# Optimization experiments

Hardware: AMD Instinct MI355X
Metric: run time of the kernel (lower is better)

Reference implementation:

```python
import jax, jax.numpy as jnp
import numpy as np

T0 = 16
EPS = 1.1920929e-07  # torch fp32 finfo eps used by F.rms_norm default

def rmsnorm(v):
    return v * jax.lax.rsqrt(jnp.mean(v * v, axis=-1, keepdims=True) + EPS)

def apply_rotary_emb(x, cos, sin):
    # x: (B, S, H, C); rotate-half style as in source
    d = x.shape[-1] // 2
    x1, x2 = x[..., :d], x[..., d:]
    return jnp.concatenate([x1 * cos + x2 * sin, -x1 * sin + x2 * cos], axis=-1)

def setup_inputs():
    key = jax.random.key(0)
    ks = jax.random.split(key, 8)
    B, T, C, H = 8, 8192, 128, 8
    S = (T0 // 4) * T0 + 1  # 64 selected tokens + 1 sink = 65
    x = jax.random.normal(ks[0], (B, T, C), jnp.float32)
    # RoPE tables over the sink-augmented attention sequence, head_dim/2 = 64
    inv = 1.0 / (10000.0 ** (jnp.arange(C // 2, dtype=jnp.float32) / (C // 2)))
    ang = jnp.arange(S, dtype=jnp.float32)[:, None] * inv[None, :]
    cos = jnp.cos(ang)[None, :, None, :]  # (1, 65, 1, 64)
    sin = jnp.sin(ang)[None, :, None, :]
    sink = 0.02 * jax.random.normal(ks[1], (1, H, C), jnp.float32)
    W_qkvg = 0.02 * jax.random.normal(ks[2], (4 * C * H, C), jnp.float32)
    patch_w = 0.02 * jax.random.normal(ks[3], (T0 * C,), jnp.float32)
    W_out = 0.02 * jax.random.normal(ks[4], (C, H * C), jnp.float32)
    tao = jnp.array([1.2, 1.2], jnp.float32)
    return {"x": x, "cos": cos, "sin": sin, "sink": sink, "W_qkvg": W_qkvg,
            "patch_w": patch_w, "W_out": W_out, "tao": tao}

def reference(x, cos, sin, sink, W_qkvg, patch_w, W_out, tao):
    B, T, C = x.shape
    H = sink.shape[1]
    Np = T // T0  # T chosen as multiple of T0, so pad P = 0
    # --- patch scoring + topk patch selection (patch_toks) ---
    xp = x.reshape(B, Np, T0 * C)
    score = jax.nn.softmax(rmsnorm(xp) @ patch_w, axis=-1)  # (B, Np)
    _, I = jax.lax.top_k(score, T0 // 4)                    # top 4 patches
    I = jnp.sort(I, axis=-1)                                # (B, 4)
    # --- qkvg projection over ALL tokens, then patch-flattened chunk ---
    qkvg = x @ W_qkvg.T                                     # (B, T, 4*C*H)
    qkvg_p = qkvg.reshape(B, Np, 4 * T0 * C * H)
    n = T0 * C * H
    q_p = qkvg_p[..., 0 * n:1 * n]
    k_p = qkvg_p[..., 1 * n:2 * n]
    v_p = qkvg_p[..., 2 * n:3 * n]
    g_p = qkvg_p[..., 3 * n:4 * n]
    def gather(p):  # (B, Np, n) -> (B, 4*T0, H, C) via selected patches
        return jnp.take_along_axis(p, I[:, :, None], axis=1).reshape(B, -1, H, C)
    q, k, v, g = gather(q_p), gather(k_p), gather(v_p), gather(g_p)
    # --- sink token prepend ---
    s = jnp.broadcast_to(sink[:, None], (B, 1, H, C))
    q = jnp.concatenate([s, q], axis=1)  # (B, 65, H, C)
    k = jnp.concatenate([s, k], axis=1)
    v = jnp.concatenate([s, v], axis=1)
    # --- RoPE + RMSNorm + learned temperatures ---
    q = rmsnorm(apply_rotary_emb(q, cos, sin)) * tao[0]
    k = rmsnorm(apply_rotary_emb(k, cos, sin)) * tao[1]
    # --- causal SDPA (scale 1/sqrt(C)), drop sink row ---
    S = q.shape[1]
    att = jnp.einsum('bshc,bthc->bhst', q, k) / jnp.sqrt(jnp.float32(C))
    causal = jnp.tril(jnp.ones((S, S), dtype=bool))
    att = jax.nn.softmax(jnp.where(causal, att, -jnp.inf), axis=-1)
    y = jnp.einsum('bhst,bthc->bshc', att, v)[:, 1:]  # (B, 64, H, C)
    # --- sigmoid gating + output projection ---
    y = y * jax.nn.sigmoid(g)
    return y.reshape(B, y.shape[1], H * C) @ W_out.T  # (B, 64, C)
```

## Files before the change

kernel.cpp:

```cpp
#include <hip/hip_runtime.h>
#include <hip/hip_bf16.h>

#define EPSR 1.1920929e-07f

#define OFF_SCORE 0LL
#define OFF_I     4096LL
#define OFF_WQT   8192LL
#define OFF_WO4   532480LL
#define OFF_SEL   663552LL
#define OFF_YG    4757504LL

__device__ __forceinline__ bool is_bf16_in(const void* tao) {
    unsigned int w = *(const unsigned int*)tao;
    return (w >> 16) == (w & 0xffffu);
}

__device__ __forceinline__ float ldin(const void* p, long long i, bool bf) {
    if (bf) return __uint_as_float(((unsigned int)(((const unsigned short*)p)[i])) << 16);
    return ((const float*)p)[i];
}

__device__ __forceinline__ float4 ldin4(const void* p, long long i, bool bf) {
    if (bf) {
        ushort4 u = ((const ushort4*)p)[i >> 2];
        return make_float4(__uint_as_float((unsigned int)u.x << 16),
                           __uint_as_float((unsigned int)u.y << 16),
                           __uint_as_float((unsigned int)u.z << 16),
                           __uint_as_float((unsigned int)u.w << 16));
    }
    return ((const float4*)p)[i >> 2];
}

__global__ __launch_bounds__(256) void k_prep_score(const void* Wq, const void* Wo,
                                                    const void* x, const void* pw,
                                                    const void* tao, float* ws) {
    bool bf = is_bf16_in(tao);
    __shared__ float tile[16448];
    int tid = threadIdx.x;
    if (blockIdx.x < 1024) {
        int lane = tid & 63, wid = tid >> 6;
        int patch = blockIdx.x * 4 + wid;
        long long base = (long long)patch * 2048;
        float ss = 0.f, dt = 0.f;
        #pragma unroll
        for (int i = 0; i < 8; i++) {
            int e = i * 256 + lane * 4;
            float4 v = ldin4(x, base + e, bf);
            float4 w = ldin4(pw, e, bf);
            ss += v.x * v.x + v.y * v.y + v.z * v.z + v.w * v.w;
            dt += v.x * w.x + v.y * w.y + v.z * w.z + v.w * w.w;
        }
        #pragma unroll
        for (int o = 32; o; o >>= 1) { ss += __shfl_xor(ss, o); dt += __shfl_xor(dt, o); }
        if (lane == 0) ws[OFF_SCORE + patch] = dt * rsqrtf(ss * (1.f / 2048.f) + EPSR);
    } else if (blockIdx.x < 1088) {
        float* WqT = ws + OFF_WQT;
        int j0 = (blockIdx.x - 1024) * 64;
        #pragma unroll
        for (int rep = 0; rep < 8; rep++) {
            int jr = rep * 8 + (tid >> 5);
            int c4 = (tid & 31) * 4;
            float4 v = ldin4(Wq, ((long long)(j0 + jr)) * 128 + c4, bf);
            float* t = &tile[jr * 129 + c4];
            t[0] = v.x; t[1] = v.y; t[2] = v.z; t[3] = v.w;
        }
        __syncthreads();
        #pragma unroll
        for (int rep = 0; rep < 8; rep++) {
            int c = rep * 16 + (tid >> 4);
            int jq = (tid & 15) * 4;
            float4 v = make_float4(tile[jq * 129 + c], tile[(jq + 1) * 129 + c],
                                   tile[(jq + 2) * 129 + c], tile[(jq + 3) * 129 + c]);
            *(float4*)&WqT[c * 4096 + j0 + jq] = v;
        }
    } else {
        float* Wo4 = ws + OFF_WO4;
        int co0 = (blockIdx.x - 1088) * 16;
        #pragma unroll
        for (int rep = 0; rep < 16; rep++) {
            float4 v = ldin4(Wo, ((long long)(co0 + rep)) * 1024 + tid * 4, bf);
            *(float4*)&tile[rep * 1028 + tid * 4] = v;
        }
        __syncthreads();
        #pragma unroll
        for (int rep = 0; rep < 16; rep++) {
            int idx = rep * 256 + tid;
            int fg = idx >> 4, co = idx & 15;
            float4 v = *(const float4*)&tile[co * 1028 + fg * 4];
            *(float4*)&Wo4[(fg * 128 + co0 + co) * 4] = v;
        }
    }
}

__global__ __launch_bounds__(64) void k_top4(float* ws) {
    const float* score = ws + OFF_SCORE;
    int* I = (int*)(ws + OFF_I);
    int b = blockIdx.x, lane = threadIdx.x;
    const float4* sp = (const float4*)(score + b * 512);
    float4 a = sp[lane * 2], c = sp[lane * 2 + 1];
    float v[8];
    v[0] = a.x; v[1] = a.y; v[2] = a.z; v[3] = a.w;
    v[4] = c.x; v[5] = c.y; v[6] = c.z; v[7] = c.w;
    int win[4];
    #pragma unroll
    for (int k = 0; k < 4; k++) {
        float bm = v[0]; int bi = 0;
        #pragma unroll
        for (int i = 1; i < 8; i++) if (v[i] > bm) { bm = v[i]; bi = i; }
        int gi = lane * 8 + bi;
        #pragma unroll
        for (int o = 32; o; o >>= 1) {
            float om = __shfl_xor(bm, o); int oi = __shfl_xor(gi, o);
            if (om > bm || (om == bm && oi < gi)) { bm = om; gi = oi; }
        }
        win[k] = gi;
        if ((gi >> 3) == lane) v[gi & 7] = -INFINITY;
    }
    if (lane == 0) {
        int a0 = win[0], a1 = win[1], a2 = win[2], a3 = win[3], tmp;
        if (a0 > a1) { tmp = a0; a0 = a1; a1 = tmp; }
        if (a2 > a3) { tmp = a2; a2 = a3; a3 = tmp; }
        if (a0 > a2) { tmp = a0; a0 = a2; a2 = tmp; }
        if (a1 > a3) { tmp = a1; a1 = a3; a3 = tmp; }
        if (a1 > a2) { tmp = a1; a1 = a2; a2 = tmp; }
        I[b * 4 + 0] = a0; I[b * 4 + 1] = a1; I[b * 4 + 2] = a2; I[b * 4 + 3] = a3;
    }
}

__global__ __launch_bounds__(128) void k_qkvg(const void* x, const void* tao, float* ws) {
    bool bf = is_bf16_in(tao);
    const int* I = (const int*)(ws + OFF_I);
    int blk = blockIdx.x;
    int jc = blk & 15, bp = blk >> 4;
    int b = bp >> 2;
    __shared__ float4 xs4[512];
    int tid = threadIdx.x;
    int tok0 = I[bp] * 16;
    long long xbase = ((long long)(b * 8192 + tok0)) * 128;
    for (int i = tid; i < 512; i += 128)
        xs4[i] = ldin4(x, xbase + i * 4, bf);
    __syncthreads();
    int ts = tid >> 6, jx = tid & 63;
    const float4* WqT4 = (const float4*)(ws + OFF_WQT);
    int wcol = jc * 64 + jx;
    float4 acc[8];
    #pragma unroll
    for (int t = 0; t < 8; t++) acc[t] = make_float4(0.f, 0.f, 0.f, 0.f);
    for (int c4 = 0; c4 < 32; c4++) {
        float4 w0 = WqT4[(c4 * 4 + 0) * 1024 + wcol];
        float4 w1 = WqT4[(c4 * 4 + 1) * 1024 + wcol];
        float4 w2 = WqT4[(c4 * 4 + 2) * 1024 + wcol];
        float4 w3 = WqT4[(c4 * 4 + 3) * 1024 + wcol];
        #pragma unroll
        for (int t = 0; t < 8; t++) {
            float4 xv = xs4[(ts * 8 + t) * 32 + c4];
            acc[t].x += xv.x * w0.x + xv.y * w1.x + xv.z * w2.x + xv.w * w3.x;
            acc[t].y += xv.x * w0.y + xv.y * w1.y + xv.z * w2.y + xv.w * w3.y;
            acc[t].z += xv.x * w0.z + xv.y * w1.z + xv.z * w2.z + xv.w * w3.z;
            acc[t].w += xv.x * w0.w + xv.y * w1.w + xv.z * w2.w + xv.w * w3.w;
        }
    }
    float4* sel4 = (float4*)(ws + OFF_SEL);
    #pragma unroll
    for (int t = 0; t < 8; t++)
        sel4[(bp * 16 + ts * 8 + t) * 1024 + wcol] = acc[t];
}

__global__ __launch_bounds__(512, 2) void k_fused(const void* sink, const void* cosp, const void* sinp,
                                                  const void* tao, float* ws) {
    bool bf = is_bf16_in(tao);
    const float* sel = ws + OFF_SEL;
    float* yg = ws + OFF_YG;
    int b = blockIdx.x >> 3, h = blockIdx.x & 7;
    int tid = threadIdx.x, lane = tid & 63, wid = tid >> 6;
    __shared__ float qs[65 * 132];
    __shared__ float ks[65 * 132];
    __shared__ float vs[65 * 132];
    __shared__ float att[65 * 68];
    float tao0 = ldin(tao, 0, bf), tao1 = ldin(tao, 1, bf);

    for (int s = wid; s < 65; s += 8) {
        float cs = ldin(cosp, s * 64 + lane, bf);
        float sn = ldin(sinp, s * 64 + lane, bf);
        #pragma unroll
        for (int which = 0; which < 3; which++) {
            float r1, r2;
            if (s == 0) {
                r1 = ldin(sink, h * 128 + lane, bf);
                r2 = ldin(sink, h * 128 + lane + 64, bf);
            } else {
                int r = s - 1, p = r >> 4, sl = r & 15;
                int tl = which * 4 + (sl >> 2);
                long long sbase = (((long long)(b * 4 + p) * 16 + tl) * 4096) + (sl & 3) * 1024 + h * 128;
                r1 = sel[sbase + lane];
                r2 = sel[sbase + lane + 64];
            }
            float o1, o2;
            if (which < 2) {
                o1 = r1 * cs + r2 * sn;
                o2 = -r1 * sn + r2 * cs;
                float ssum = o1 * o1 + o2 * o2;
                #pragma unroll
                for (int o = 32; o; o >>= 1) ssum += __shfl_xor(ssum, o);
                float sc = rsqrtf(ssum * (1.f / 128.f) + EPSR) * (which == 0 ? tao0 : tao1);
                o1 *= sc; o2 *= sc;
            } else {
                o1 = r1; o2 = r2;
            }
            float* dst = (which == 0 ? qs : which == 1 ? ks : vs);
            dst[s * 132 + lane] = o1;
            dst[s * 132 + lane + 64] = o2;
        }
    }
    __syncthreads();

    for (int tile = tid; tile < 561; tile += 512) {
        int u = tile, sT = 0;
        while (u >= sT + 1) { u -= sT + 1; sT++; }
        int tT = u;
        int s0 = sT * 2, t0 = tT * 2;
        const float* q0 = &qs[s0 * 132];
        const float* q1 = &qs[(s0 + 1 > 64 ? 64 : s0 + 1) * 132];
        const float* k0 = &ks[t0 * 132];
        const float* k1 = &ks[(t0 + 1 > 64 ? 64 : t0 + 1) * 132];
        float a00 = 0.f, a01 = 0.f, a10 = 0.f, a11 = 0.f;
        #pragma unroll 4
        for (int c = 0; c < 128; c += 4) {
            float4 qa = *(const float4*)(q0 + c);
            float4 qb = *(const float4*)(q1 + c);
            float4 ka = *(const float4*)(k0 + c);
            float4 kb = *(const float4*)(k1 + c);
            a00 += qa.x * ka.x + qa.y * ka.y + qa.z * ka.z + qa.w * ka.w;
            a01 += qa.x * kb.x + qa.y * kb.y + qa.z * kb.z + qa.w * kb.w;
            a10 += qb.x * ka.x + qb.y * ka.y + qb.z * ka.z + qb.w * ka.w;
            a11 += qb.x * kb.x + qb.y * kb.y + qb.z * kb.z + qb.w * kb.w;
        }
        const float scale = 0.08838834764831845f;
        if (t0 <= s0)                          att[s0 * 68 + t0] = a00 * scale;
        if (t0 + 1 <= s0)                      att[s0 * 68 + t0 + 1] = a01 * scale;
        if (s0 + 1 <= 64 && t0 <= s0 + 1)      att[(s0 + 1) * 68 + t0] = a10 * scale;
        if (s0 + 1 <= 64 && t0 + 1 <= s0 + 1)  att[(s0 + 1) * 68 + t0 + 1] = a11 * scale;
    }
    __syncthreads();

    for (int s = wid; s < 65; s += 8) {
        float x1 = (lane <= s) ? __expf(att[s * 68 + lane]) : 0.f;
        float x2 = (lane == 0 && s == 64) ? __expf(att[s * 68 + 64]) : 0.f;
        float sum = x1 + x2;
        #pragma unroll
        for (int o = 32; o; o >>= 1) sum += __shfl_xor(sum, o);
        float inv = 1.f / sum;
        att[s * 68 + lane] = x1 * inv;
        if (lane < 4) att[s * 68 + 64 + lane] = (lane == 0) ? x2 * inv : 0.f;
    }
    __syncthreads();

    {
        int rt = tid >> 4, ct = tid & 15;
        int c0 = ct * 8;
        float acc[2][8];
        #pragma unroll
        for (int i = 0; i < 2; i++)
            #pragma unroll
            for (int j = 0; j < 8; j++) acc[i][j] = 0.f;
        const float* ar[2];
        #pragma unroll
        for (int i = 0; i < 2; i++) ar[i] = &att[(1 + rt * 2 + i) * 68];
        for (int t4 = 0; t4 < 64; t4 += 4) {
            float aw[2][4];
            #pragma unroll
            for (int i = 0; i < 2; i++) *(float4*)aw[i] = *(const float4*)(ar[i] + t4);
            #pragma unroll
            for (int j = 0; j < 4; j++) {
                const float* vp = &vs[(t4 + j) * 132 + c0];
                float4 v1 = *(const float4*)vp;
                float4 v2 = *(const float4*)(vp + 4);
                #pragma unroll
                for (int i = 0; i < 2; i++) {
                    float a = aw[i][j];
                    acc[i][0] += a * v1.x; acc[i][1] += a * v1.y;
                    acc[i][2] += a * v1.z; acc[i][3] += a * v1.w;
                    acc[i][4] += a * v2.x; acc[i][5] += a * v2.y;
                    acc[i][6] += a * v2.z; acc[i][7] += a * v2.w;
                }
            }
        }
        {
            const float* vp = &vs[64 * 132 + c0];
            float4 v1 = *(const float4*)vp;
            float4 v2 = *(const float4*)(vp + 4);
            #pragma unroll
            for (int i = 0; i < 2; i++) {
                float a = ar[i][64];
                acc[i][0] += a * v1.x; acc[i][1] += a * v1.y;
                acc[i][2] += a * v1.z; acc[i][3] += a * v1.w;
                acc[i][4] += a * v2.x; acc[i][5] += a * v2.y;
                acc[i][6] += a * v2.z; acc[i][7] += a * v2.w;
            }
        }
        #pragma unroll
        for (int i = 0; i < 2; i++) {
            int r = rt * 2 + i;
            int p = r >> 4, sl = r & 15, tl = 12 + (sl >> 2);
            long long gb = (((long long)(b * 4 + p) * 16 + tl) * 4096) + (sl & 3) * 1024 + h * 128 + c0;
            float4 g1 = *(const float4*)&sel[gb];
            float4 g2 = *(const float4*)&sel[gb + 4];
            float4 o1, o2;
            o1.x = acc[i][0] / (1.f + __expf(-g1.x));
            o1.y = acc[i][1] / (1.f + __expf(-g1.y));
            o1.z = acc[i][2] / (1.f + __expf(-g1.z));
            o1.w = acc[i][3] / (1.f + __expf(-g1.w));
            o2.x = acc[i][4] / (1.f + __expf(-g2.x));
            o2.y = acc[i][5] / (1.f + __expf(-g2.y));
            o2.z = acc[i][6] / (1.f + __expf(-g2.z));
            o2.w = acc[i][7] / (1.f + __expf(-g2.w));
            long long yb = ((long long)(b * 64 + r)) * 1024 + h * 128 + c0;
            *(float4*)&yg[yb] = o1;
            *(float4*)&yg[yb + 4] = o2;
        }
    }
}

__global__ __launch_bounds__(256) void k_out(const void* tao, float* ws, void* out) {
    bool bf = is_bf16_in(tao);
    int blk = blockIdx.x;
    int b = blk >> 5, r0 = (blk & 31) * 2;
    __shared__ float4 ygs4[512];
    __shared__ float part[512];
    int tid = threadIdx.x;
    const float4* yg4 = (const float4*)(ws + OFF_YG);
    for (int i = tid; i < 512; i += 256) {
        int row = i >> 8, f4 = i & 255;
        ygs4[i] = yg4[(b * 64 + r0 + row) * 256 + f4];
    }
    __syncthreads();
    int co = tid & 127, fs = tid >> 7;
    const float4* Wo44 = (const float4*)(ws + OFF_WO4);
    float a0 = 0.f, a1 = 0.f;
    int g0 = fs * 128;
    #pragma unroll 2
    for (int g = g0; g < g0 + 128; g++) {
        float4 w = Wo44[g * 128 + co];
        float4 y0 = ygs4[g];
        float4 y1 = ygs4[256 + g];
        a0 += w.x * y0.x + w.y * y0.y + w.z * y0.z + w.w * y0.w;
        a1 += w.x * y1.x + w.y * y1.y + w.z * y1.z + w.w * y1.w;
    }
    part[fs * 256 + co] = a0;
    part[fs * 256 + 128 + co] = a1;
    __syncthreads();
    int row = tid >> 7;
    float v = part[row * 128 + co] + part[256 + row * 128 + co];
    long long o = ((long long)(b * 64 + r0 + row)) * 128 + co;
    if (bf) ((__hip_bfloat16*)out)[o] = __float2bfloat16(v);
    else    ((float*)out)[o] = v;
}

extern "C" void kernel_launch(void* const* d_in, const int* in_sizes, int n_in,
                              void* d_out, int out_size, void* d_ws, size_t ws_size,
                              hipStream_t stream) {
    const void* x    = d_in[0];
    const void* cosp = d_in[1];
    const void* sinp = d_in[2];
    const void* sink = d_in[3];
    const void* Wq   = d_in[4];
    const void* pw   = d_in[5];
    const void* Wo   = d_in[6];
    const void* tao  = d_in[7];
    float* ws = (float*)d_ws;

    k_prep_score<<<dim3(1096), dim3(256), 0, stream>>>(Wq, Wo, x, pw, tao, ws);
    k_top4 <<<dim3(8), dim3(64), 0, stream>>>(ws);
    k_qkvg <<<dim3(512), dim3(128), 0, stream>>>(x, tao, ws);
    k_fused<<<dim3(64), dim3(512), 0, stream>>>(sink, cosp, sinp, tao, ws);
    k_out  <<<dim3(256), dim3(256), 0, stream>>>(tao, ws, d_out);
}
```

Measured before the change: 165.9 us.

## Fuse top-4 into qkvg kernel and split attention by query quarter

```diff
diff --git a/kernel.cpp b/kernel.cpp
--- a/kernel.cpp
+++ b/kernel.cpp
@@ -4,7 +4,6 @@
 #define EPSR 1.1920929e-07f
 
 #define OFF_SCORE 0LL
-#define OFF_I     4096LL
 #define OFF_WQT   8192LL
 #define OFF_WO4   532480LL
 #define OFF_SEL   663552LL
@@ -92,68 +91,73 @@
     }
 }
 
-__global__ __launch_bounds__(64) void k_top4(float* ws) {
-    const float* score = ws + OFF_SCORE;
-    int* I = (int*)(ws + OFF_I);
-    int b = blockIdx.x, lane = threadIdx.x;
-    const float4* sp = (const float4*)(score + b * 512);
-    float4 a = sp[lane * 2], c = sp[lane * 2 + 1];
-    float v[8];
-    v[0] = a.x; v[1] = a.y; v[2] = a.z; v[3] = a.w;
-    v[4] = c.x; v[5] = c.y; v[6] = c.z; v[7] = c.w;
-    int win[4];
-    #pragma unroll
-    for (int k = 0; k < 4; k++) {
-        float bm = v[0]; int bi = 0;
-        #pragma unroll
-        for (int i = 1; i < 8; i++) if (v[i] > bm) { bm = v[i]; bi = i; }
-        int gi = lane * 8 + bi;
-        #pragma unroll
-        for (int o = 32; o; o >>= 1) {
-            float om = __shfl_xor(bm, o); int oi = __shfl_xor(gi, o);
-            if (om > bm || (om == bm && oi < gi)) { bm = om; gi = oi; }
-        }
-        win[k] = gi;
-        if ((gi >> 3) == lane) v[gi & 7] = -INFINITY;
-    }
-    if (lane == 0) {
-        int a0 = win[0], a1 = win[1], a2 = win[2], a3 = win[3], tmp;
-        if (a0 > a1) { tmp = a0; a0 = a1; a1 = tmp; }
-        if (a2 > a3) { tmp = a2; a2 = a3; a3 = tmp; }
-        if (a0 > a2) { tmp = a0; a0 = a2; a2 = tmp; }
-        if (a1 > a3) { tmp = a1; a1 = a3; a3 = tmp; }
-        if (a1 > a2) { tmp = a1; a1 = a2; a2 = tmp; }
-        I[b * 4 + 0] = a0; I[b * 4 + 1] = a1; I[b * 4 + 2] = a2; I[b * 4 + 3] = a3;
-    }
-}
-
-__global__ __launch_bounds__(128) void k_qkvg(const void* x, const void* tao, float* ws) {
+__global__ __launch_bounds__(256) void k_qkvg(const void* x, const void* tao, float* ws) {
     bool bf = is_bf16_in(tao);
-    const int* I = (const int*)(ws + OFF_I);
     int blk = blockIdx.x;
     int jc = blk & 15, bp = blk >> 4;
-    int b = bp >> 2;
+    int b = bp >> 2, p = bp & 3;
     __shared__ float4 xs4[512];
+    __shared__ int tok0s;
     int tid = threadIdx.x;
-    int tok0 = I[bp] * 16;
+    if (tid < 64) {
+        const float4* sp = (const float4*)(ws + OFF_SCORE + b * 512);
+        float4 a = sp[tid * 2], c = sp[tid * 2 + 1];
+        float v[8];
+        v[0] = a.x; v[1] = a.y; v[2] = a.z; v[3] = a.w;
+        v[4] = c.x; v[5] = c.y; v[6] = c.z; v[7] = c.w;
+        int win[4];
+        #pragma unroll
+        for (int k = 0; k < 4; k++) {
+            float bm = v[0]; int bi = 0;
+            #pragma unroll
+            for (int i = 1; i < 8; i++) if (v[i] > bm) { bm = v[i]; bi = i; }
+            int gi = tid * 8 + bi;
+            #pragma unroll
+            for (int o = 32; o; o >>= 1) {
+                float om = __shfl_xor(bm, o); int oi = __shfl_xor(gi, o);
+                if (om > bm || (om == bm && oi < gi)) { bm = om; gi = oi; }
+            }
+            win[k] = gi;
+            if ((gi >> 3) == tid) v[gi & 7] = -INFINITY;
+        }
+        if (tid == 0) {
+            int a0 = win[0], a1 = win[1], a2 = win[2], a3 = win[3], tmp;
+            if (a0 > a1) { tmp = a0; a0 = a1; a1 = tmp; }
+            if (a2 > a3) { tmp = a2; a2 = a3; a3 = tmp; }
+            if (a0 > a2) { tmp = a0; a0 = a2; a2 = tmp; }
+            if (a1 > a3) { tmp = a1; a1 = a3; a3 = tmp; }
+            if (a1 > a2) { tmp = a1; a1 = a2; a2 = tmp; }
+            int sorted[4] = {a0, a1, a2, a3};
+            tok0s = sorted[p] * 16;
+        }
+    }
+    __syncthreads();
+    int tok0 = tok0s;
     long long xbase = ((long long)(b * 8192 + tok0)) * 128;
-    for (int i = tid; i < 512; i += 128)
+    for (int i = tid; i < 512; i += 256)
         xs4[i] = ldin4(x, xbase + i * 4, bf);
     __syncthreads();
-    int ts = tid >> 6, jx = tid & 63;
+    int tg = tid >> 6, jx = tid & 63;
     const float4* WqT4 = (const float4*)(ws + OFF_WQT);
     int wcol = jc * 64 + jx;
-    float4 acc[8];
+    float4 acc[4];
     #pragma unroll
-    for (int t = 0; t < 8; t++) acc[t] = make_float4(0.f, 0.f, 0.f, 0.f);
+    for (int t = 0; t < 4; t++) acc[t] = make_float4(0.f, 0.f, 0.f, 0.f);
+    float4 nw0 = WqT4[0 * 1024 + wcol];
+    float4 nw1 = WqT4[1 * 1024 + wcol];
+    float4 nw2 = WqT4[2 * 1024 + wcol];
+    float4 nw3 = WqT4[3 * 1024 + wcol];
     for (int c4 = 0; c4 < 32; c4++) {
-        float4 w0 = WqT4[(c4 * 4 + 0) * 1024 + wcol];
-        float4 w1 = WqT4[(c4 * 4 + 1) * 1024 + wcol];
-        float4 w2 = WqT4[(c4 * 4 + 2) * 1024 + wcol];
-        float4 w3 = WqT4[(c4 * 4 + 3) * 1024 + wcol];
-        #pragma unroll
-        for (int t = 0; t < 8; t++) {
-            float4 xv = xs4[(ts * 8 + t) * 32 + c4];
+        float4 w0 = nw0, w1 = nw1, w2 = nw2, w3 = nw3;
+        if (c4 < 31) {
+            nw0 = WqT4[(c4 * 4 + 4) * 1024 + wcol];
+            nw1 = WqT4[(c4 * 4 + 5) * 1024 + wcol];
+            nw2 = WqT4[(c4 * 4 + 6) * 1024 + wcol];
+            nw3 = WqT4[(c4 * 4 + 7) * 1024 + wcol];
+        }
+        #pragma unroll
+        for (int t = 0; t < 4; t++) {
+            float4 xv = xs4[(tg * 4 + t) * 32 + c4];
             acc[t].x += xv.x * w0.x + xv.y * w1.x + xv.z * w2.x + xv.w * w3.x;
             acc[t].y += xv.x * w0.y + xv.y * w1.y + xv.z * w2.y + xv.w * w3.y;
             acc[t].z += xv.x * w0.z + xv.y * w1.z + xv.z * w2.z + xv.w * w3.z;
@@ -162,8 +166,8 @@
     }
     float4* sel4 = (float4*)(ws + OFF_SEL);
     #pragma unroll
-    for (int t = 0; t < 8; t++)
-        sel4[(bp * 16 + ts * 8 + t) * 1024 + wcol] = acc[t];
+    for (int t = 0; t < 4; t++)
+        sel4[(bp * 16 + tg * 4 + t) * 1024 + wcol] = acc[t];
 }
 
 __global__ __launch_bounds__(512, 2) void k_fused(const void* sink, const void* cosp, const void* sinp,
@@ -171,27 +175,31 @@
     bool bf = is_bf16_in(tao);
     const float* sel = ws + OFF_SEL;
     float* yg = ws + OFF_YG;
-    int b = blockIdx.x >> 3, h = blockIdx.x & 7;
+    int blk = blockIdx.x;
+    int b = blk >> 5, h = (blk >> 2) & 7, qd = blk & 3;
+    int bp = b * 4 + qd;
+    int smax = qd * 16 + 16;
     int tid = threadIdx.x, lane = tid & 63, wid = tid >> 6;
-    __shared__ float qs[65 * 132];
+    __shared__ float qs[16 * 132];
     __shared__ float ks[65 * 132];
     __shared__ float vs[65 * 132];
-    __shared__ float att[65 * 68];
+    __shared__ float att[16 * 68];
     float tao0 = ldin(tao, 0, bf), tao1 = ldin(tao, 1, bf);
 
-    for (int s = wid; s < 65; s += 8) {
+    for (int s = wid; s <= smax; s += 8) {
         float cs = ldin(cosp, s * 64 + lane, bf);
         float sn = ldin(sinp, s * 64 + lane, bf);
         #pragma unroll
         for (int which = 0; which < 3; which++) {
+            if (which == 0 && !(s > qd * 16)) continue;
             float r1, r2;
             if (s == 0) {
                 r1 = ldin(sink, h * 128 + lane, bf);
                 r2 = ldin(sink, h * 128 + lane + 64, bf);
             } else {
-                int r = s - 1, p = r >> 4, sl = r & 15;
+                int r = s - 1, pp = r >> 4, sl = r & 15;
                 int tl = which * 4 + (sl >> 2);
-                long long sbase = (((long long)(b * 4 + p) * 16 + tl) * 4096) + (sl & 3) * 1024 + h * 128;
+                long long sbase = (((long long)(b * 4 + pp) * 16 + tl) * 4096) + (sl & 3) * 1024 + h * 128;
                 r1 = sel[sbase + lane];
                 r2 = sel[sbase + lane + 64];
             }
@@ -207,117 +215,96 @@
             } else {
                 o1 = r1; o2 = r2;
             }
-            float* dst = (which == 0 ? qs : which == 1 ? ks : vs);
-            dst[s * 132 + lane] = o1;
-            dst[s * 132 + lane + 64] = o2;
-        }
-    }
-    __syncthreads();
-
-    for (int tile = tid; tile < 561; tile += 512) {
-        int u = tile, sT = 0;
-        while (u >= sT + 1) { u -= sT + 1; sT++; }
-        int tT = u;
-        int s0 = sT * 2, t0 = tT * 2;
-        const float* q0 = &qs[s0 * 132];
-        const float* q1 = &qs[(s0 + 1 > 64 ? 64 : s0 + 1) * 132];
-        const float* k0 = &ks[t0 * 132];
-        const float* k1 = &ks[(t0 + 1 > 64 ? 64 : t0 + 1) * 132];
-        float a00 = 0.f, a01 = 0.f, a10 = 0.f, a11 = 0.f;
-        #pragma unroll 4
-        for (int c = 0; c < 128; c += 4) {
-            float4 qa = *(const float4*)(q0 + c);
-            float4 qb = *(const float4*)(q1 + c);
-            float4 ka = *(const float4*)(k0 + c);
-            float4 kb = *(const float4*)(k1 + c);
-            a00 += qa.x * ka.x + qa.y * ka.y + qa.z * ka.z + qa.w * ka.w;
-            a01 += qa.x * kb.x + qa.y * kb.y + qa.z * kb.z + qa.w * kb.w;
-            a10 += qb.x * ka.x + qb.y * ka.y + qb.z * ka.z + qb.w * ka.w;
-            a11 += qb.x * kb.x + qb.y * kb.y + qb.z * kb.z + qb.w * kb.w;
-        }
-        const float scale = 0.08838834764831845f;
-        if (t0 <= s0)                          att[s0 * 68 + t0] = a00 * scale;
-        if (t0 + 1 <= s0)                      att[s0 * 68 + t0 + 1] = a01 * scale;
-        if (s0 + 1 <= 64 && t0 <= s0 + 1)      att[(s0 + 1) * 68 + t0] = a10 * scale;
-        if (s0 + 1 <= 64 && t0 + 1 <= s0 + 1)  att[(s0 + 1) * 68 + t0 + 1] = a11 * scale;
-    }
-    __syncthreads();
-
-    for (int s = wid; s < 65; s += 8) {
-        float x1 = (lane <= s) ? __expf(att[s * 68 + lane]) : 0.f;
-        float x2 = (lane == 0 && s == 64) ? __expf(att[s * 68 + 64]) : 0.f;
+            float* dst;
+            int row;
+            if (which == 0)      { dst = qs; row = s - qd * 16 - 1; }
+            else if (which == 1) { dst = ks; row = s; }
+            else                 { dst = vs; row = s; }
+            dst[row * 132 + lane] = o1;
+            dst[row * 132 + lane + 64] = o2;
+        }
+    }
+    __syncthreads();
+
+    {
+        int ttiles = qd * 8 + 9;
+        int ntiles = 8 * ttiles;
+        if (tid < ntiles) {
+            int sT = tid & 7, tT = tid >> 3;
+            int ls0 = sT * 2;
+            int s0g = qd * 16 + 1 + ls0;
+            int t0 = tT * 2;
+            if (t0 <= s0g + 1) {
+                int t1 = (t0 + 1 > smax) ? smax : t0 + 1;
+                const float* q0 = &qs[ls0 * 132];
+                const float* q1 = &qs[(ls0 + 1) * 132];
+                const float* k0 = &ks[t0 * 132];
+                const float* k1 = &ks[t1 * 132];
+                float a00 = 0.f, a01 = 0.f, a10 = 0.f, a11 = 0.f;
+                #pragma unroll 4
+                for (int c = 0; c < 128; c += 4) {
+                    float4 qa = *(const float4*)(q0 + c);
+                    float4 qb = *(const float4*)(q1 + c);
+                    float4 ka = *(const float4*)(k0 + c);
+                    float4 kb = *(const float4*)(k1 + c);
+                    a00 += qa.x * ka.x + qa.y * ka.y + qa.z * ka.z + qa.w * ka.w;
+                    a01 += qa.x * kb.x + qa.y * kb.y + qa.z * kb.z + qa.w * kb.w;
+                    a10 += qb.x * ka.x + qb.y * ka.y + qb.z * ka.z + qb.w * ka.w;
+                    a11 += qb.x * kb.x + qb.y * kb.y + qb.z * kb.z + qb.w * kb.w;
+                }
+                const float scale = 0.08838834764831845f;
+                if (t0 <= s0g)         att[ls0 * 68 + t0] = a00 * scale;
+                if (t0 + 1 <= s0g)     att[ls0 * 68 + t0 + 1] = a01 * scale;
+                if (t0 <= s0g + 1)     att[(ls0 + 1) * 68 + t0] = a10 * scale;
+                if (t0 + 1 <= s0g + 1) att[(ls0 + 1) * 68 + t0 + 1] = a11 * scale;
+            }
+        }
+    }
+    __syncthreads();
+
+    for (int ls = wid; ls < 16; ls += 8) {
+        int s = qd * 16 + 1 + ls;
+        float x1 = (lane <= s) ? __expf(att[ls * 68 + lane]) : 0.f;
+        float x2 = (lane == 0 && s == 64) ? __expf(att[ls * 68 + 64]) : 0.f;
         float sum = x1 + x2;
         #pragma unroll
         for (int o = 32; o; o >>= 1) sum += __shfl_xor(sum, o);
         float inv = 1.f / sum;
-        att[s * 68 + lane] = x1 * inv;
-        if (lane < 4) att[s * 68 + 64 + lane] = (lane == 0) ? x2 * inv : 0.f;
+        att[ls * 68 + lane] = x1 * inv;
+        if (lane < 4) att[ls * 68 + 64 + lane] = (lane == 0) ? x2 * inv : 0.f;
     }
     __syncthreads();
 
     {
-        int rt = tid >> 4, ct = tid & 15;
-        int c0 = ct * 8;
-        float acc[2][8];
-        #pragma unroll
-        for (int i = 0; i < 2; i++)
-            #pragma unroll
-            for (int j = 0; j < 8; j++) acc[i][j] = 0.f;
-        const float* ar[2];
-        #pragma unroll
-        for (int i = 0; i < 2; i++) ar[i] = &att[(1 + rt * 2 + i) * 68];
-        for (int t4 = 0; t4 < 64; t4 += 4) {
-            float aw[2][4];
-            #pragma unroll
-            for (int i = 0; i < 2; i++) *(float4*)aw[i] = *(const float4*)(ar[i] + t4);
-            #pragma unroll
-            for (int j = 0; j < 4; j++) {
-                const float* vp = &vs[(t4 + j) * 132 + c0];
-                float4 v1 = *(const float4*)vp;
-                float4 v2 = *(const float4*)(vp + 4);
-                #pragma unroll
-                for (int i = 0; i < 2; i++) {
-                    float a = aw[i][j];
-                    acc[i][0] += a * v1.x; acc[i][1] += a * v1.y;
-                    acc[i][2] += a * v1.z; acc[i][3] += a * v1.w;
-                    acc[i][4] += a * v2.x; acc[i][5] += a * v2.y;
-                    acc[i][6] += a * v2.z; acc[i][7] += a * v2.w;
-                }
-            }
+        int row = tid >> 5, c0 = (tid & 31) * 4;
+        float4 acc = make_float4(0.f, 0.f, 0.f, 0.f);
+        const float* ar = &att[row * 68];
+        for (int t4 = 0; t4 < smax; t4 += 4) {
+            float4 aw = *(const float4*)(ar + t4);
+            float4 v0 = *(const float4*)&vs[(t4 + 0) * 132 + c0];
+            float4 v1 = *(const float4*)&vs[(t4 + 1) * 132 + c0];
+            float4 v2 = *(const float4*)&vs[(t4 + 2) * 132 + c0];
+            float4 v3 = *(const float4*)&vs[(t4 + 3) * 132 + c0];
+            acc.x += aw.x * v0.x + aw.y * v1.x + aw.z * v2.x + aw.w * v3.x;
+            acc.y += aw.x * v0.y + aw.y * v1.y + aw.z * v2.y + aw.w * v3.y;
+            acc.z += aw.x * v0.z + aw.y * v1.z + aw.z * v2.z + aw.w * v3.z;
+            acc.w += aw.x * v0.w + aw.y * v1.w + aw.z * v2.w + aw.w * v3.w;
         }
         {
-            const float* vp = &vs[64 * 132 + c0];
-            float4 v1 = *(const float4*)vp;
-            float4 v2 = *(const float4*)(vp + 4);
-            #pragma unroll
-            for (int i = 0; i < 2; i++) {
-                float a = ar[i][64];
-                acc[i][0] += a * v1.x; acc[i][1] += a * v1.y;
-                acc[i][2] += a * v1.z; acc[i][3] += a * v1.w;
-                acc[i][4] += a * v2.x; acc[i][5] += a * v2.y;
-                acc[i][6] += a * v2.z; acc[i][7] += a * v2.w;
-            }
-        }
-        #pragma unroll
-        for (int i = 0; i < 2; i++) {
-            int r = rt * 2 + i;
-            int p = r >> 4, sl = r & 15, tl = 12 + (sl >> 2);
-            long long gb = (((long long)(b * 4 + p) * 16 + tl) * 4096) + (sl & 3) * 1024 + h * 128 + c0;
-            float4 g1 = *(const float4*)&sel[gb];
-            float4 g2 = *(const float4*)&sel[gb + 4];
-            float4 o1, o2;
-            o1.x = acc[i][0] / (1.f + __expf(-g1.x));
-            o1.y = acc[i][1] / (1.f + __expf(-g1.y));
-            o1.z = acc[i][2] / (1.f + __expf(-g1.z));
-            o1.w = acc[i][3] / (1.f + __expf(-g1.w));
-            o2.x = acc[i][4] / (1.f + __expf(-g2.x));
-            o2.y = acc[i][5] / (1.f + __expf(-g2.y));
-            o2.z = acc[i][6] / (1.f + __expf(-g2.z));
-            o2.w = acc[i][7] / (1.f + __expf(-g2.w));
-            long long yb = ((long long)(b * 64 + r)) * 1024 + h * 128 + c0;
-            *(float4*)&yg[yb] = o1;
-            *(float4*)&yg[yb + 4] = o2;
-        }
+            float a = ar[smax];
+            float4 vt = *(const float4*)&vs[smax * 132 + c0];
+            acc.x += a * vt.x; acc.y += a * vt.y; acc.z += a * vt.z; acc.w += a * vt.w;
+        }
+        int r = qd * 16 + row;
+        int sl = row, tl = 12 + (sl >> 2);
+        long long gb = (((long long)bp * 16 + tl) * 4096) + (sl & 3) * 1024 + h * 128 + c0;
+        float4 g = *(const float4*)&sel[gb];
+        acc.x /= (1.f + __expf(-g.x));
+        acc.y /= (1.f + __expf(-g.y));
+        acc.z /= (1.f + __expf(-g.z));
+        acc.w /= (1.f + __expf(-g.w));
+        long long yb = ((long long)(b * 64 + r)) * 1024 + h * 128 + c0;
+        *(float4*)&yg[yb] = acc;
     }
 }
 
@@ -370,8 +357,7 @@
     float* ws = (float*)d_ws;
 
     k_prep_score<<<dim3(1096), dim3(256), 0, stream>>>(Wq, Wo, x, pw, tao, ws);
-    k_top4 <<<dim3(8), dim3(64), 0, stream>>>(ws);
-    k_qkvg <<<dim3(512), dim3(128), 0, stream>>>(x, tao, ws);
-    k_fused<<<dim3(64), dim3(512), 0, stream>>>(sink, cosp, sinp, tao, ws);
+    k_qkvg <<<dim3(512), dim3(256), 0, stream>>>(x, tao, ws);
+    k_fused<<<dim3(256), dim3(512), 0, stream>>>(sink, cosp, sinp, tao, ws);
     k_out  <<<dim3(256), dim3(256), 0, stream>>>(tao, ws, d_out);
 }
```

Result: faster. 147.3 us (-11.2%).
